# Optimization experiments

Measured on AMD Instinct MI355X. Metric: run time of the kernel, lower is better.

The kernel has to match this reference:

```python
import jax, jax.numpy as jnp
import numpy as np
from jax import lax

CHUNK = 128
EPS = 1e-6


def rmsnorm(x, w, eps=EPS):
    var = jnp.mean(jnp.square(x.astype(jnp.float32)), axis=-1, keepdims=True)
    return (x * lax.rsqrt(var + eps)).astype(x.dtype) * w


def linear_attn(q, k, v, slopes):
    """Decay-based (lightning/RetNet-style) causal linear attention.
    q,k,v: [B,H,S,D]; slopes: [H,1,1] positive per-head decay rates.
    out[i] = sum_{j<=i} exp(-s*(i-j)) * (q_i . k_j) * v_j, via chunked scan.
    """
    B, H, S, D = q.shape
    C = CHUNK
    nC = S // C
    s = slopes.reshape(1, H, 1, 1).astype(jnp.float32)  # [1,H,1,1]
    t = jnp.arange(C, dtype=jnp.float32)
    q_dec = jnp.exp(-s * t[None, None, :, None])            # [1,H,C,1] decay for inter-chunk query
    k_dec = jnp.exp(-s * (C - t)[None, None, :, None])      # [1,H,C,1] decay applied to keys entering state
    chunk_dec = jnp.exp(-s * C)                              # [1,H,1,1] whole-chunk state decay
    rel = t[:, None] - t[None, :]                            # [C,C]
    intra_dec = jnp.where(rel >= 0, jnp.exp(-s * rel), 0.0)  # [1,H,C,C] causal intra-chunk decay

    # [nC,B,H,C,D]
    qc = q.reshape(B, H, nC, C, D).transpose(2, 0, 1, 3, 4)
    kc = k.reshape(B, H, nC, C, D).transpose(2, 0, 1, 3, 4)
    vc = v.reshape(B, H, nC, C, D).transpose(2, 0, 1, 3, 4)

    def step(kv, inp):
        qi, ki, vi = inp  # each [B,H,C,D]; kv: [B,H,D,D]
        inter = jnp.einsum('bhcd,bhde->bhce', qi * q_dec, kv)
        scores = jnp.einsum('bhcd,bhed->bhce', qi, ki) * intra_dec  # [B,H,C,C]
        intra = jnp.einsum('bhce,bhed->bhcd', scores, vi)
        kv_new = chunk_dec * kv + jnp.einsum('bhcd,bhce->bhde', ki * k_dec, vi)
        return kv_new, inter + intra

    kv0 = jnp.zeros((B, H, D, D), dtype=jnp.float32)
    _, out = lax.scan(step, kv0, (qc, kc, vc))  # out: [nC,B,H,C,D]
    return out.transpose(1, 2, 0, 3, 4).reshape(B, H, S, D)


def setup_inputs() -> dict:
    key = jax.random.key(0)
    ks = jax.random.split(key, 8)
    B, S, E, H, D = 2, 2048, 2048, 16, 128
    init = 0.02
    hidden_states = jax.random.normal(ks[0], (B, S, E), dtype=jnp.float32)
    attention_mask = jnp.ones((B, S), dtype=jnp.float32)
    # standard ALiBi-like per-head slopes in (0,1]
    slope_rate = (2.0 ** (-8.0 * (jnp.arange(H, dtype=jnp.float32) + 1.0) / H)).reshape(H, 1, 1)
    Wq = jax.random.normal(ks[1], (E, H * D), dtype=jnp.float32) * init
    Wk = jax.random.normal(ks[2], (E, H * D), dtype=jnp.float32) * init
    Wv = jax.random.normal(ks[3], (E, H * D), dtype=jnp.float32) * init
    Wg = jax.random.normal(ks[4], (E, H * D), dtype=jnp.float32) * init
    Wo = jax.random.normal(ks[5], (H * D, E), dtype=jnp.float32) * init
    norm_w = jnp.ones((H * D,), dtype=jnp.float32)
    return {"hidden_states": hidden_states, "attention_mask": attention_mask,
            "slope_rate": slope_rate, "Wq": Wq, "Wk": Wk, "Wv": Wv,
            "Wg": Wg, "Wo": Wo, "norm_w": norm_w}


def reference(hidden_states, attention_mask, slope_rate, Wq, Wk, Wv, Wg, Wo, norm_w):
    B, S, E = hidden_states.shape
    H = slope_rate.shape[0]
    D = Wq.shape[1] // H
    q = (hidden_states @ Wq).reshape(B, S, H, D).transpose(0, 2, 1, 3)
    k = (hidden_states @ Wk).reshape(B, S, H, D).transpose(0, 2, 1, 3)
    v = (hidden_states @ Wv).reshape(B, S, H, D).transpose(0, 2, 1, 3)
    v = v * attention_mask[:, None, :, None]
    out = linear_attn(q, k, v, slope_rate)                      # [B,H,S,D]
    out = out.transpose(0, 2, 1, 3).reshape(B, S, H * D)        # b h n d -> b n (h d)
    out = rmsnorm(out, norm_w)
    out = jax.nn.sigmoid(hidden_states @ Wg) * out
    return out @ Wo
```

## Files before the change

### kernel.cpp

```cpp
#include <hip/hip_runtime.h>
#include <cstdint>
#include <cstddef>

typedef unsigned short u16;
typedef unsigned int   u32;

#define SEQ    2048
#define EDIM   2048
#define HEADS  16
#define DHEAD  128
#define CCH    128
#define NCH    16
#define TOKENS 4096

typedef __attribute__((ext_vector_type(8))) short short8;
typedef __attribute__((ext_vector_type(4))) float floatx4;

__device__ __forceinline__ float b2f(u16 b) {
    u32 u = ((u32)b) << 16; float f; __builtin_memcpy(&f, &u, 4); return f;
}
__device__ __forceinline__ u16 f2b(float f) {
    u32 u; __builtin_memcpy(&u, &f, 4);
    u32 r = (u + 0x7fffu + ((u >> 16) & 1u)) >> 16;
    return (u16)r;
}
__device__ __forceinline__ void unpack8(uint4 u, float* f) {
    f[0] = b2f((u16)(u.x & 0xffff)); f[1] = b2f((u16)(u.x >> 16));
    f[2] = b2f((u16)(u.y & 0xffff)); f[3] = b2f((u16)(u.y >> 16));
    f[4] = b2f((u16)(u.z & 0xffff)); f[5] = b2f((u16)(u.z >> 16));
    f[6] = b2f((u16)(u.w & 0xffff)); f[7] = b2f((u16)(u.w >> 16));
}
__device__ __forceinline__ uint4 pack8(const float* f) {
    uint4 u;
    u.x = (u32)f2b(f[0]) | ((u32)f2b(f[1]) << 16);
    u.y = (u32)f2b(f[2]) | ((u32)f2b(f[3]) << 16);
    u.z = (u32)f2b(f[4]) | ((u32)f2b(f[5]) << 16);
    u.w = (u32)f2b(f[6]) | ((u32)f2b(f[7]) << 16);
    return u;
}

__device__ __forceinline__ void gld_lds16(const u16* g, u16* l) {
    __builtin_amdgcn_global_load_lds((const __attribute__((address_space(1))) void*)g,
                                     (__attribute__((address_space(3))) void*)l, 16, 0, 0);
}

__global__ __launch_bounds__(256) void k_f32_to_bf16(const float* __restrict__ in,
                                                     u16* __restrict__ out) {
    int i = blockIdx.x * 256 + threadIdx.x;
    float4 v = ((const float4*)in)[i];
    uint2 o;
    o.x = (u32)f2b(v.x) | ((u32)f2b(v.y) << 16);
    o.y = (u32)f2b(v.z) | ((u32)f2b(v.w) << 16);
    ((uint2*)out)[i] = o;
}

__global__ void k_transW(const float* __restrict__ W0, const float* __restrict__ W1,
                         const float* __restrict__ W2, const float* __restrict__ W3,
                         const float* __restrict__ W4, u16* __restrict__ out) {
    const float* W;
    int z = blockIdx.z;
    switch (z) {
        case 0: W = W0; break; case 1: W = W1; break; case 2: W = W2; break;
        case 3: W = W3; break; default: W = W4; break;
    }
    __shared__ float tile[32][33];
    int n = blockIdx.x * 32 + threadIdx.x;
    int k = blockIdx.y * 32 + threadIdx.y;
    tile[threadIdx.y][threadIdx.x] = W[(size_t)k * EDIM + n];
    __syncthreads();
    int on = blockIdx.x * 32 + threadIdx.y;
    int ok = blockIdx.y * 32 + threadIdx.x;
    out[(size_t)z * EDIM * EDIM + (size_t)on * EDIM + ok] = f2b(tile[threadIdx.x][threadIdx.y]);
}

__global__ __launch_bounds__(256) void k_gemm(const u16* __restrict__ A,
                                              const u16* __restrict__ Bt,
                                              void* __restrict__ C,
                                              int K, int N,
                                              long long zstrB, long long zstrC,
                                              int out_bf16) {
    __shared__ u16 As[128 * 32];
    __shared__ u16 Bs[128 * 32];
    const u16* Bz = Bt + (size_t)blockIdx.z * (size_t)zstrB;
    int m0 = blockIdx.y * 128, n0 = blockIdx.x * 128;
    int tid = threadIdx.x;
    int w = tid >> 6, lane = tid & 63;
    int wr = w >> 1, wc = w & 1;
    int lrow = lane & 15, khalf = lane >> 4;

    floatx4 acc[4][4];
#pragma unroll
    for (int i = 0; i < 4; i++)
#pragma unroll
        for (int j = 0; j < 4; j++) acc[i][j] = (floatx4){0.f, 0.f, 0.f, 0.f};

    int c0 = tid, c1 = tid + 256;
    int r0 = c0 >> 2, p0 = (c0 & 3) * 8;
    int r1 = c1 >> 2, p1 = (c1 & 3) * 8;
    const u16* a0 = A  + (size_t)(m0 + r0) * K + p0;
    const u16* a1 = A  + (size_t)(m0 + r1) * K + p1;
    const u16* b0 = Bz + (size_t)(n0 + r0) * K + p0;
    const u16* b1 = Bz + (size_t)(n0 + r1) * K + p1;

    for (int k0 = 0; k0 < K; k0 += 32) {
        gld_lds16(a0 + k0, &As[c0 * 8]);
        gld_lds16(a1 + k0, &As[c1 * 8]);
        gld_lds16(b0 + k0, &Bs[c0 * 8]);
        gld_lds16(b1 + k0, &Bs[c1 * 8]);
        __syncthreads();
        short8 af[4], bfr[4];
#pragma unroll
        for (int i = 0; i < 4; i++)
            af[i] = *(const short8*)&As[(wr * 64 + i * 16 + lrow) * 32 + khalf * 8];
#pragma unroll
        for (int j = 0; j < 4; j++)
            bfr[j] = *(const short8*)&Bs[(wc * 64 + j * 16 + lrow) * 32 + khalf * 8];
#pragma unroll
        for (int i = 0; i < 4; i++)
#pragma unroll
            for (int j = 0; j < 4; j++)
                acc[i][j] = __builtin_amdgcn_mfma_f32_16x16x32_bf16(af[i], bfr[j], acc[i][j], 0, 0, 0);
        __syncthreads();
    }

    size_t cz = (size_t)blockIdx.z * (size_t)zstrC;
#pragma unroll
    for (int i = 0; i < 4; i++)
#pragma unroll
        for (int j = 0; j < 4; j++) {
            int mrow = m0 + wr * 64 + i * 16 + khalf * 4;
            int ncol = n0 + wc * 64 + j * 16 + lrow;
#pragma unroll
            for (int r = 0; r < 4; r++) {
                float val = acc[i][j][r];
                if (out_bf16)
                    ((u16*)C)[cz + (size_t)(mrow + r) * N + ncol] = f2b(val);
                else
                    ((float*)C)[cz + (size_t)(mrow + r) * N + ncol] = val;
            }
        }
}

__global__ __launch_bounds__(256) void k_transT(const u16* __restrict__ kin,
                                                const u16* __restrict__ vin,
                                                const float* __restrict__ mask,
                                                const float* __restrict__ slopes,
                                                u16* __restrict__ KdT,
                                                u16* __restrict__ VT) {
    __shared__ u16 T[128 * 136];
    int bid = blockIdx.x;
    int isK = blockIdx.y;
    int c = bid & 15, h = (bid >> 4) & 15, b = bid >> 8;
    int tid = threadIdx.x;
    size_t tokbase = (size_t)(b * SEQ + c * CCH);
    const u16* src = (isK ? kin : vin) + tokbase * EDIM + h * DHEAD;
    float s = slopes[h];
#pragma unroll
    for (int i = 0; i < 8; i++) {
        int cidx = tid + i * 256;
        int t = cidx >> 4, part = (cidx & 15) * 8;
        float sc = isK ? expf(-s * (float)(CCH - t)) : mask[(size_t)b * SEQ + c * CCH + t];
        float f[8]; unpack8(*(const uint4*)(src + (size_t)t * EDIM + part), f);
#pragma unroll
        for (int j = 0; j < 8; j++) f[j] *= sc;
        *(uint4*)&T[t * 136 + part] = pack8(f);
    }
    __syncthreads();
    int e = tid >> 1, t0 = (tid & 1) * 64;
    u16* dst = (isK ? KdT : VT) + (size_t)bid * 16384 + (size_t)e * 128 + t0;
#pragma unroll
    for (int blk = 0; blk < 8; blk++) {
        u16 v8[8];
#pragma unroll
        for (int j = 0; j < 8; j++) v8[j] = T[(t0 + blk * 8 + j) * 136 + e];
        *(uint4*)(dst + blk * 8) = *(uint4*)v8;
    }
}

__global__ __launch_bounds__(256) void k_kvc(const u16* __restrict__ VT,
                                             const u16* __restrict__ KdT,
                                             u16* __restrict__ kvT) {
    int bid = blockIdx.x, tid = threadIdx.x;
    int w = tid >> 6, lane = tid & 63;
    int wr = w >> 1, wc = w & 1;
    int lrow = lane & 15, khalf = lane >> 4;
    const u16* va = VT  + (size_t)bid * 16384;
    const u16* kb = KdT + (size_t)bid * 16384;
    floatx4 acc[4][4];
#pragma unroll
    for (int i = 0; i < 4; i++)
#pragma unroll
        for (int j = 0; j < 4; j++) acc[i][j] = (floatx4){0.f, 0.f, 0.f, 0.f};
#pragma unroll
    for (int kk = 0; kk < 4; kk++) {
        short8 a[4], bf[4];
#pragma unroll
        for (int i = 0; i < 4; i++)
            a[i] = *(const short8*)(va + (size_t)(wr * 64 + i * 16 + lrow) * 128 + kk * 32 + khalf * 8);
#pragma unroll
        for (int j = 0; j < 4; j++)
            bf[j] = *(const short8*)(kb + (size_t)(wc * 64 + j * 16 + lrow) * 128 + kk * 32 + khalf * 8);
#pragma unroll
        for (int i = 0; i < 4; i++)
#pragma unroll
            for (int j = 0; j < 4; j++)
                acc[i][j] = __builtin_amdgcn_mfma_f32_16x16x32_bf16(a[i], bf[j], acc[i][j], 0, 0, 0);
    }
    u16* o = kvT + (size_t)bid * 16384;
#pragma unroll
    for (int i = 0; i < 4; i++)
#pragma unroll
        for (int j = 0; j < 4; j++)
#pragma unroll
            for (int r = 0; r < 4; r++)
                o[(size_t)(wr * 64 + i * 16 + khalf * 4 + r) * 128 + wc * 64 + j * 16 + lrow] =
                    f2b(acc[i][j][r]);
}

__global__ __launch_bounds__(256) void k_scan(u16* __restrict__ kvbuf,
                                              const float* __restrict__ slopes) {
    int gid = blockIdx.x * 256 + threadIdx.x;
    int idx = gid & 16383;
    int bh = gid >> 14;
    int h = bh & 15;
    float cd = expf(-slopes[h] * (float)CCH);
    u16* p = kvbuf + (size_t)bh * NCH * 16384 + idx;
    float st = 0.f;
    for (int c = 0; c < NCH; c++) {
        float tmp = b2f(p[(size_t)c * 16384]);
        p[(size_t)c * 16384] = f2b(st);
        st = cd * st + tmp;
    }
}

__global__ __launch_bounds__(256) void k_attn_out(const u16* __restrict__ q,
                                                  const u16* __restrict__ k,
                                                  const u16* __restrict__ VT,
                                                  const u16* __restrict__ kvT,
                                                  const float* __restrict__ slopes,
                                                  u16* __restrict__ attn) {
    __shared__ u16 KS[128 * 136];
    int bid = blockIdx.x;
    int c = bid & 15, h = (bid >> 4) & 15, b = bid >> 8;
    float s = slopes[h];
    int tid = threadIdx.x;
    int w = tid >> 6, lane = tid & 63;
    int wr = w >> 1, wc = w & 1;
    int lrow = lane & 15, khalf = lane >> 4;
    size_t tokbase = (size_t)(b * SEQ + c * CCH);

    {
        const u16* kg = k + tokbase * EDIM + h * DHEAD;
#pragma unroll
        for (int i = 0; i < 8; i++) {
            int cidx = tid + i * 256;
            int t = cidx >> 4, part = (cidx & 15) * 8;
            *(uint4*)&KS[t * 136 + part] = *(const uint4*)(kg + (size_t)t * EDIM + part);
        }
    }
    short8 qa[4][4];
    {
        const u16* qgbase = q + tokbase * EDIM + h * DHEAD;
#pragma unroll
        for (int i = 0; i < 4; i++) {
            const u16* qrow = qgbase + (size_t)(wr * 64 + i * 16 + lrow) * EDIM;
#pragma unroll
            for (int kk = 0; kk < 4; kk++)
                qa[i][kk] = *(const short8*)(qrow + kk * 32 + khalf * 8);
        }
    }
    __syncthreads();

    floatx4 acc[4][4];
#pragma unroll
    for (int i = 0; i < 4; i++)
#pragma unroll
        for (int j = 0; j < 4; j++) acc[i][j] = (floatx4){0.f, 0.f, 0.f, 0.f};
#pragma unroll
    for (int kk = 0; kk < 4; kk++) {
        short8 bf[4];
#pragma unroll
        for (int j = 0; j < 4; j++)
            bf[j] = *(const short8*)&KS[(wc * 64 + j * 16 + lrow) * 136 + kk * 32 + khalf * 8];
#pragma unroll
        for (int i = 0; i < 4; i++)
#pragma unroll
            for (int j = 0; j < 4; j++)
                acc[i][j] = __builtin_amdgcn_mfma_f32_16x16x32_bf16(qa[i][kk], bf[j], acc[i][j], 0, 0, 0);
    }
    __syncthreads();

#pragma unroll
    for (int i = 0; i < 4; i++)
#pragma unroll
        for (int j = 0; j < 4; j++) {
            int tbase = wr * 64 + i * 16 + khalf * 4;
            int u = wc * 64 + j * 16 + lrow;
#pragma unroll
            for (int r = 0; r < 4; r++) {
                int t = tbase + r;
                float val = (t >= u) ? acc[i][j][r] * expf(-s * (float)(t - u)) : 0.f;
                KS[t * 136 + u] = f2b(val);
            }
        }
    __syncthreads();

#pragma unroll
    for (int i = 0; i < 4; i++)
#pragma unroll
        for (int j = 0; j < 4; j++) acc[i][j] = (floatx4){0.f, 0.f, 0.f, 0.f};
    const u16* st = kvT + (size_t)bid * 16384;
#pragma unroll
    for (int kk = 0; kk < 4; kk++) {
        short8 bf[4];
#pragma unroll
        for (int j = 0; j < 4; j++)
            bf[j] = *(const short8*)(st + (size_t)(wc * 64 + j * 16 + lrow) * 128 + kk * 32 + khalf * 8);
#pragma unroll
        for (int i = 0; i < 4; i++)
#pragma unroll
            for (int j = 0; j < 4; j++)
                acc[i][j] = __builtin_amdgcn_mfma_f32_16x16x32_bf16(qa[i][kk], bf[j], acc[i][j], 0, 0, 0);
    }
#pragma unroll
    for (int i = 0; i < 4; i++)
#pragma unroll
        for (int r = 0; r < 4; r++) {
            float qd = expf(-s * (float)(wr * 64 + i * 16 + khalf * 4 + r));
#pragma unroll
            for (int j = 0; j < 4; j++) acc[i][j][r] *= qd;
        }
    const u16* vt = VT + (size_t)bid * 16384;
#pragma unroll
    for (int kk = 0; kk < 4; kk++) {
        short8 sa[4], bf[4];
#pragma unroll
        for (int i = 0; i < 4; i++)
            sa[i] = *(const short8*)&KS[(wr * 64 + i * 16 + lrow) * 136 + kk * 32 + khalf * 8];
#pragma unroll
        for (int j = 0; j < 4; j++)
            bf[j] = *(const short8*)(vt + (size_t)(wc * 64 + j * 16 + lrow) * 128 + kk * 32 + khalf * 8);
#pragma unroll
        for (int i = 0; i < 4; i++)
#pragma unroll
            for (int j = 0; j < 4; j++)
                acc[i][j] = __builtin_amdgcn_mfma_f32_16x16x32_bf16(sa[i], bf[j], acc[i][j], 0, 0, 0);
    }

    u16* og = attn + tokbase * EDIM + h * DHEAD;
#pragma unroll
    for (int i = 0; i < 4; i++)
#pragma unroll
        for (int j = 0; j < 4; j++)
#pragma unroll
            for (int r = 0; r < 4; r++)
                og[(size_t)(wr * 64 + i * 16 + khalf * 4 + r) * EDIM + wc * 64 + j * 16 + lrow] =
                    f2b(acc[i][j][r]);
}

__global__ __launch_bounds__(256) void k_rms_gate(const u16* __restrict__ attn,
                                                  const u16* __restrict__ gpre,
                                                  const float* __restrict__ nw,
                                                  u16* __restrict__ out) {
    int n = blockIdx.x, tid = threadIdx.x;
    float a[8];
    unpack8(((const uint4*)(attn + (size_t)n * EDIM))[tid], a);
    float ss = 0.f;
#pragma unroll
    for (int j = 0; j < 8; j++) ss += a[j] * a[j];
#pragma unroll
    for (int o = 32; o > 0; o >>= 1) ss += __shfl_down(ss, o, 64);
    __shared__ float red[5];
    int w = tid >> 6, lane = tid & 63;
    if (lane == 0) red[w] = ss;
    __syncthreads();
    if (tid == 0) red[4] = rsqrtf((red[0] + red[1] + red[2] + red[3]) / 2048.f + 1e-6f);
    __syncthreads();
    float rs = red[4];
    float g[8];
    unpack8(((const uint4*)(gpre + (size_t)n * EDIM))[tid], g);
    const float4* np4 = (const float4*)(nw + tid * 8);
    float4 w0 = np4[0], w1 = np4[1];
    float wv[8] = {w0.x, w0.y, w0.z, w0.w, w1.x, w1.y, w1.z, w1.w};
    float o8[8];
#pragma unroll
    for (int j = 0; j < 8; j++) {
        float sg = 1.f / (1.f + expf(-g[j]));
        o8[j] = sg * (a[j] * rs * wv[j]);
    }
    ((uint4*)(out + (size_t)n * EDIM))[tid] = pack8(o8);
}

extern "C" void kernel_launch(void* const* d_in, const int* in_sizes, int n_in,
                              void* d_out, int out_size, void* d_ws, size_t ws_size,
                              hipStream_t stream) {
    const float* hs     = (const float*)d_in[0];
    const float* mask   = (const float*)d_in[1];
    const float* slopes = (const float*)d_in[2];
    const float* Wq     = (const float*)d_in[3];
    const float* Wk     = (const float*)d_in[4];
    const float* Wv     = (const float*)d_in[5];
    const float* Wg     = (const float*)d_in[6];
    const float* Wo     = (const float*)d_in[7];
    const float* nw     = (const float*)d_in[8];
    float* out = (float*)d_out;

    char* ws = (char*)d_ws;
    u16* hsb   = (u16*)ws;
    u16* Wt    = (u16*)(ws + 16777216LL);
    u16* qkvg  = (u16*)(ws + 58720256LL);
    u16* kvbuf = (u16*)(ws + 125829120LL);
    u16* attn  = (u16*)(ws + 142606336LL);
    u16* VT  = hsb;
    u16* KdT = attn;

    k_f32_to_bf16<<<8192, 256, 0, stream>>>(hs, hsb);
    k_transW<<<dim3(64, 64, 5), dim3(32, 32, 1), 0, stream>>>(Wq, Wk, Wv, Wg, Wo, Wt);
    k_gemm<<<dim3(16, 32, 4), 256, 0, stream>>>(hsb, Wt, qkvg, EDIM, EDIM,
                                                (long long)EDIM * EDIM,
                                                (long long)TOKENS * EDIM, 1);
    u16* qb = qkvg;
    u16* kb = qkvg + 8388608LL;
    u16* vb = qkvg + 16777216LL;
    u16* gb = qkvg + 25165824LL;
    k_transT<<<dim3(512, 2), 256, 0, stream>>>(kb, vb, mask, slopes, KdT, VT);
    k_kvc<<<512, 256, 0, stream>>>(VT, KdT, kvbuf);
    k_scan<<<2048, 256, 0, stream>>>(kvbuf, slopes);
    k_attn_out<<<512, 256, 0, stream>>>(qb, kb, VT, kvbuf, slopes, attn);
    k_rms_gate<<<TOKENS, 256, 0, stream>>>(attn, gb, nw, hsb);
    k_gemm<<<dim3(16, 32, 1), 256, 0, stream>>>(hsb, Wt + 4LL * 4194304LL, out, EDIM, EDIM,
                                                0LL, 0LL, 0);
}
```

Baseline: 493.8 us.

## Fuse K/V transpose-scale into projection GEMM epilogue and widen K tile with swizzled LDS

Removes the separate k_transT kernel by having the QKVG GEMM epilogue write decay-scaled transposed K and mask-scaled transposed V tiles directly. V is written only in transposed form, and its buffer is placed where the plain V output used to go. The GEMM K-step is doubled to 64, with an XOR-swizzled LDS layout to avoid bank conflicts, which halves the number of barriers per K loop. Several expf calls become fast __expf. The risks are higher LDS use, which may lower occupancy, scattered 8-byte transposed stores in the epilogue, and slightly reduced exp precision.

```diff
diff --git a/kernel.cpp b/kernel.cpp
--- a/kernel.cpp
+++ b/kernel.cpp
@@ -78,10 +78,15 @@
                                               void* __restrict__ C,
                                               int K, int N,
                                               long long zstrB, long long zstrC,
-                                              int out_bf16) {
-    __shared__ u16 As[128 * 32];
-    __shared__ u16 Bs[128 * 32];
-    const u16* Bz = Bt + (size_t)blockIdx.z * (size_t)zstrB;
+                                              int out_bf16, int mode,
+                                              u16* __restrict__ KdT,
+                                              u16* __restrict__ VT,
+                                              const float* __restrict__ slopes,
+                                              const float* __restrict__ mask) {
+    __shared__ u16 As[128 * 64];
+    __shared__ u16 Bs[128 * 64];
+    int z = blockIdx.z;
+    const u16* Bz = Bt + (size_t)z * (size_t)zstrB;
     int m0 = blockIdx.y * 128, n0 = blockIdx.x * 128;
     int tid = threadIdx.x;
     int w = tid >> 6, lane = tid & 63;
@@ -94,86 +99,93 @@
 #pragma unroll
         for (int j = 0; j < 4; j++) acc[i][j] = (floatx4){0.f, 0.f, 0.f, 0.f};
 
-    int c0 = tid, c1 = tid + 256;
-    int r0 = c0 >> 2, p0 = (c0 & 3) * 8;
-    int r1 = c1 >> 2, p1 = (c1 & 3) * 8;
-    const u16* a0 = A  + (size_t)(m0 + r0) * K + p0;
-    const u16* a1 = A  + (size_t)(m0 + r1) * K + p1;
-    const u16* b0 = Bz + (size_t)(n0 + r0) * K + p0;
-    const u16* b1 = Bz + (size_t)(n0 + r1) * K + p1;
-
-    for (int k0 = 0; k0 < K; k0 += 32) {
-        gld_lds16(a0 + k0, &As[c0 * 8]);
-        gld_lds16(a1 + k0, &As[c1 * 8]);
-        gld_lds16(b0 + k0, &Bs[c0 * 8]);
-        gld_lds16(b1 + k0, &Bs[c1 * 8]);
+    const u16* aptr[4];
+    const u16* bptr[4];
+#pragma unroll
+    for (int i = 0; i < 4; i++) {
+        int c = tid + i * 256;
+        int row = c >> 3, slot = c & 7;
+        int g = slot ^ (row & 7);
+        aptr[i] = A  + (size_t)(m0 + row) * K + g * 8;
+        bptr[i] = Bz + (size_t)(n0 + row) * K + g * 8;
+    }
+    int aoff[2][4], boff[2][4];
+#pragma unroll
+    for (int kk = 0; kk < 2; kk++)
+#pragma unroll
+        for (int i = 0; i < 4; i++) {
+            int ra = wr * 64 + i * 16 + lrow;
+            int rb = wc * 64 + i * 16 + lrow;
+            int gg = kk * 4 + khalf;
+            aoff[kk][i] = ra * 64 + ((gg ^ (ra & 7)) * 8);
+            boff[kk][i] = rb * 64 + ((gg ^ (rb & 7)) * 8);
+        }
+
+    for (int k0 = 0; k0 < K; k0 += 64) {
+#pragma unroll
+        for (int i = 0; i < 4; i++) {
+            gld_lds16(aptr[i] + k0, &As[(tid + i * 256) * 8]);
+            gld_lds16(bptr[i] + k0, &Bs[(tid + i * 256) * 8]);
+        }
         __syncthreads();
-        short8 af[4], bfr[4];
-#pragma unroll
-        for (int i = 0; i < 4; i++)
-            af[i] = *(const short8*)&As[(wr * 64 + i * 16 + lrow) * 32 + khalf * 8];
-#pragma unroll
-        for (int j = 0; j < 4; j++)
-            bfr[j] = *(const short8*)&Bs[(wc * 64 + j * 16 + lrow) * 32 + khalf * 8];
-#pragma unroll
-        for (int i = 0; i < 4; i++)
-#pragma unroll
-            for (int j = 0; j < 4; j++)
-                acc[i][j] = __builtin_amdgcn_mfma_f32_16x16x32_bf16(af[i], bfr[j], acc[i][j], 0, 0, 0);
+#pragma unroll
+        for (int kk = 0; kk < 2; kk++) {
+            short8 af[4], bfr[4];
+#pragma unroll
+            for (int i = 0; i < 4; i++) af[i]  = *(const short8*)&As[aoff[kk][i]];
+#pragma unroll
+            for (int j = 0; j < 4; j++) bfr[j] = *(const short8*)&Bs[boff[kk][j]];
+#pragma unroll
+            for (int i = 0; i < 4; i++)
+#pragma unroll
+                for (int j = 0; j < 4; j++)
+                    acc[i][j] = __builtin_amdgcn_mfma_f32_16x16x32_bf16(af[i], bfr[j], acc[i][j], 0, 0, 0);
+        }
         __syncthreads();
     }
 
-    size_t cz = (size_t)blockIdx.z * (size_t)zstrC;
-#pragma unroll
-    for (int i = 0; i < 4; i++)
-#pragma unroll
-        for (int j = 0; j < 4; j++) {
-            int mrow = m0 + wr * 64 + i * 16 + khalf * 4;
-            int ncol = n0 + wc * 64 + j * 16 + lrow;
-#pragma unroll
-            for (int r = 0; r < 4; r++) {
-                float val = acc[i][j][r];
-                if (out_bf16)
-                    ((u16*)C)[cz + (size_t)(mrow + r) * N + ncol] = f2b(val);
-                else
-                    ((float*)C)[cz + (size_t)(mrow + r) * N + ncol] = val;
+    int writeVT  = (mode == 1 && z == 2);
+    int writeKdT = (mode == 1 && z == 1);
+
+    if (!writeVT) {
+        size_t cz = (size_t)z * (size_t)zstrC;
+#pragma unroll
+        for (int i = 0; i < 4; i++)
+#pragma unroll
+            for (int j = 0; j < 4; j++) {
+                int mrow = m0 + wr * 64 + i * 16 + khalf * 4;
+                int ncol = n0 + wc * 64 + j * 16 + lrow;
+#pragma unroll
+                for (int r = 0; r < 4; r++) {
+                    float val = acc[i][j][r];
+                    if (out_bf16)
+                        ((u16*)C)[cz + (size_t)(mrow + r) * N + ncol] = f2b(val);
+                    else
+                        ((float*)C)[cz + (size_t)(mrow + r) * N + ncol] = val;
+                }
             }
-        }
-}
-
-__global__ __launch_bounds__(256) void k_transT(const u16* __restrict__ kin,
-                                                const u16* __restrict__ vin,
-                                                const float* __restrict__ mask,
-                                                const float* __restrict__ slopes,
-                                                u16* __restrict__ KdT,
-                                                u16* __restrict__ VT) {
-    __shared__ u16 T[128 * 136];
-    int bid = blockIdx.x;
-    int isK = blockIdx.y;
-    int c = bid & 15, h = (bid >> 4) & 15, b = bid >> 8;
-    int tid = threadIdx.x;
-    size_t tokbase = (size_t)(b * SEQ + c * CCH);
-    const u16* src = (isK ? kin : vin) + tokbase * EDIM + h * DHEAD;
-    float s = slopes[h];
-#pragma unroll
-    for (int i = 0; i < 8; i++) {
-        int cidx = tid + i * 256;
-        int t = cidx >> 4, part = (cidx & 15) * 8;
-        float sc = isK ? expf(-s * (float)(CCH - t)) : mask[(size_t)b * SEQ + c * CCH + t];
-        float f[8]; unpack8(*(const uint4*)(src + (size_t)t * EDIM + part), f);
-#pragma unroll
-        for (int j = 0; j < 8; j++) f[j] *= sc;
-        *(uint4*)&T[t * 136 + part] = pack8(f);
-    }
-    __syncthreads();
-    int e = tid >> 1, t0 = (tid & 1) * 64;
-    u16* dst = (isK ? KdT : VT) + (size_t)bid * 16384 + (size_t)e * 128 + t0;
-#pragma unroll
-    for (int blk = 0; blk < 8; blk++) {
-        u16 v8[8];
-#pragma unroll
-        for (int j = 0; j < 8; j++) v8[j] = T[(t0 + blk * 8 + j) * 136 + e];
-        *(uint4*)(dst + blk * 8) = *(uint4*)v8;
+    }
+    if (writeVT || writeKdT) {
+        int b = blockIdx.y >> 4, cc = blockIdx.y & 15, h = blockIdx.x;
+        size_t tile = ((size_t)b * 256 + (size_t)h * 16 + (size_t)cc) * 16384;
+        float s = slopes[h];
+        u16* dst = (writeVT ? VT : KdT) + tile;
+#pragma unroll
+        for (int i = 0; i < 4; i++)
+#pragma unroll
+            for (int j = 0; j < 4; j++) {
+                int t0 = wr * 64 + i * 16 + khalf * 4;
+                int d  = wc * 64 + j * 16 + lrow;
+                u16 pk[4];
+#pragma unroll
+                for (int r = 0; r < 4; r++) {
+                    int t = t0 + r;
+                    float sc = writeVT ? mask[(size_t)b * SEQ + cc * CCH + t]
+                                       : __expf(-s * (float)(CCH - t));
+                    pk[r] = f2b(acc[i][j][r] * sc);
+                }
+                *(uint2*)&dst[(size_t)d * 128 + t0] = *(const uint2*)pk;
+            }
     }
 }
 
@@ -223,7 +235,7 @@
     int idx = gid & 16383;
     int bh = gid >> 14;
     int h = bh & 15;
-    float cd = expf(-slopes[h] * (float)CCH);
+    float cd = __expf(-slopes[h] * (float)CCH);
     u16* p = kvbuf + (size_t)bh * NCH * 16384 + idx;
     float st = 0.f;
     for (int c = 0; c < NCH; c++) {
@@ -299,7 +311,7 @@
 #pragma unroll
             for (int r = 0; r < 4; r++) {
                 int t = tbase + r;
-                float val = (t >= u) ? acc[i][j][r] * expf(-s * (float)(t - u)) : 0.f;
+                float val = (t >= u) ? acc[i][j][r] * __expf(-s * (float)(t - u)) : 0.f;
                 KS[t * 136 + u] = f2b(val);
             }
         }
@@ -326,7 +338,7 @@
     for (int i = 0; i < 4; i++)
 #pragma unroll
         for (int r = 0; r < 4; r++) {
-            float qd = expf(-s * (float)(wr * 64 + i * 16 + khalf * 4 + r));
+            float qd = __expf(-s * (float)(wr * 64 + i * 16 + khalf * 4 + r));
 #pragma unroll
             for (int j = 0; j < 4; j++) acc[i][j][r] *= qd;
         }
@@ -385,7 +397,7 @@
     float o8[8];
 #pragma unroll
     for (int j = 0; j < 8; j++) {
-        float sg = 1.f / (1.f + expf(-g[j]));
+        float sg = 1.f / (1.f + __expf(-g[j]));
         o8[j] = sg * (a[j] * rs * wv[j]);
     }
     ((uint4*)(out + (size_t)n * EDIM))[tid] = pack8(o8);
@@ -411,23 +423,23 @@
     u16* qkvg  = (u16*)(ws + 58720256LL);
     u16* kvbuf = (u16*)(ws + 125829120LL);
     u16* attn  = (u16*)(ws + 142606336LL);
-    u16* VT  = hsb;
+    u16* qb  = qkvg;
+    u16* kb  = qkvg + 8388608LL;
+    u16* VT  = qkvg + 16777216LL;
+    u16* gb  = qkvg + 25165824LL;
     u16* KdT = attn;
 
     k_f32_to_bf16<<<8192, 256, 0, stream>>>(hs, hsb);
     k_transW<<<dim3(64, 64, 5), dim3(32, 32, 1), 0, stream>>>(Wq, Wk, Wv, Wg, Wo, Wt);
     k_gemm<<<dim3(16, 32, 4), 256, 0, stream>>>(hsb, Wt, qkvg, EDIM, EDIM,
                                                 (long long)EDIM * EDIM,
-                                                (long long)TOKENS * EDIM, 1);
-    u16* qb = qkvg;
-    u16* kb = qkvg + 8388608LL;
-    u16* vb = qkvg + 16777216LL;
-    u16* gb = qkvg + 25165824LL;
-    k_transT<<<dim3(512, 2), 256, 0, stream>>>(kb, vb, mask, slopes, KdT, VT);
+                                                (long long)TOKENS * EDIM, 1,
+                                                1, KdT, VT, slopes, mask);
     k_kvc<<<512, 256, 0, stream>>>(VT, KdT, kvbuf);
     k_scan<<<2048, 256, 0, stream>>>(kvbuf, slopes);
     k_attn_out<<<512, 256, 0, stream>>>(qb, kb, VT, kvbuf, slopes, attn);
     k_rms_gate<<<TOKENS, 256, 0, stream>>>(attn, gb, nw, hsb);
     k_gemm<<<dim3(16, 32, 1), 256, 0, stream>>>(hsb, Wt + 4LL * 4194304LL, out, EDIM, EDIM,
-                                                0LL, 0LL, 0);
-}
+                                                0LL, 0LL, 0,
+                                                0, (u16*)nullptr, (u16*)nullptr, slopes, mask);
+}
```

New measurement: 458.1 us. -7.2%, faster.
